# Optimization experiments

Measured on AMD Instinct MI355X. Metric: run time of the kernel, lower is better.

## Reference

```python
import jax, jax.numpy as jnp
import numpy as np

B, S, DIN, DOUT = 4, 2048, 4096, 4096

def setup_inputs() -> dict:
    key = jax.random.key(0)
    k1, k2, k3, k4 = jax.random.split(key, 4)
    x = jax.random.normal(k1, (B, S, DIN), dtype=jnp.float32)
    # int8 per-channel quantized weight (stored here as int32 holding int8 range values)
    weight = jax.random.randint(k2, (DOUT, DIN), -127, 128, dtype=jnp.int32)
    weight_scale = jax.random.uniform(k3, (DOUT,), dtype=jnp.float32, minval=0.001, maxval=0.02)
    weight_offset = jax.random.randint(k4, (DOUT,), -8, 8, dtype=jnp.int32)
    return {"x": x, "weight": weight, "weight_scale": weight_scale, "weight_offset": weight_offset}

def reference(x, weight, weight_scale, weight_offset):
    # W8A16 weight-only dequant: per-output-channel (w - offset) * scale, then GEMM.
    w_fp = (weight.astype(x.dtype) - weight_offset.astype(x.dtype)[:, None]) * weight_scale.astype(x.dtype)[:, None]  # [DOUT, DIN]
    # [B,S,DIN] @ [DOUT,DIN]^T -> [B,S,DOUT]
    return jnp.einsum('bsd,od->bso', x, w_fp)
```

## Files before the change

### kernel.cpp

```cpp
#include <hip/hip_runtime.h>
#include <stdint.h>

#define DIN   4096
#define DOUT  4096
#define MTOT  8192
#define NT    64

#define BM    256
#define BN    256
#define GRID_M (MTOT / BM)
#define GRID_N (DOUT / BN)
#define NWG   (GRID_M * GRID_N)

typedef __attribute__((ext_vector_type(4)))  float        f32x4;
typedef __attribute__((ext_vector_type(16))) float        f32x16;
typedef __attribute__((ext_vector_type(4)))  int          i32x4;
typedef __attribute__((ext_vector_type(4)))  unsigned int u32x4;
typedef __attribute__((ext_vector_type(2)))  unsigned int u32x2;
typedef __attribute__((ext_vector_type(8)))  short        bf16x8;

__device__ __forceinline__ unsigned int pack_bf2_rne(float a, float b) {
  unsigned int ua = __builtin_bit_cast(unsigned int, a);
  unsigned int ub = __builtin_bit_cast(unsigned int, b);
  ua += 0x7fffu + ((ua >> 16) & 1u);
  ub += 0x7fffu + ((ub >> 16) & 1u);
  return (ua >> 16) | (ub & 0xffff0000u);
}

__device__ __forceinline__ unsigned int pack_bf2_exact(int a, int b) {
  unsigned int ua = __builtin_bit_cast(unsigned int, (float)a);
  unsigned int ub = __builtin_bit_cast(unsigned int, (float)b);
  return (ua >> 16) | (ub & 0xffff0000u);
}

#define UNITS_A (GRID_M * 2 * NT)
#define UNITS_B (GRID_N * 2 * NT)
__global__ __launch_bounds__(256) void conv_kernel(const float* __restrict__ X,
                                                   u32x4* __restrict__ wsA,
                                                   const int* __restrict__ W,
                                                   const int* __restrict__ Off,
                                                   u32x4* __restrict__ wsB) {
  const int totA = UNITS_A * 1024;
  const int totB = UNITS_B * 1024;
  for (int idx = blockIdx.x * 256 + threadIdx.x; idx < totA + totB;
       idx += gridDim.x * 256) {
    if (idx < totA) {
      const int pos = idx & 1023;
      const int row = pos >> 3, ch = pos & 7;
      const int unit = idx >> 10;
      const int kt = unit & (NT - 1), rb = unit >> 6;
      const int m = rb * 128 + row;
      const f32x4* src = (const f32x4*)(X + ((long)m << 12) + kt * 64 + ch * 8);
      f32x4 f0 = src[0], f1 = src[1];
      u32x4 d;
      d[0] = pack_bf2_rne(f0[0], f0[1]);
      d[1] = pack_bf2_rne(f0[2], f0[3]);
      d[2] = pack_bf2_rne(f1[0], f1[1]);
      d[3] = pack_bf2_rne(f1[2], f1[3]);
      wsA[(long)unit * 1024 + ch * 128 + row] = d;
    } else {
      const int j = idx - totA;
      const int pos = j & 1023;
      const int row = pos >> 3, ch = pos & 7;
      const int unit = j >> 10;
      const int kt = unit & (NT - 1), nb = unit >> 6;
      const int n = nb * 128 + row;
      const i32x4* src = (const i32x4*)(W + ((long)n << 12) + kt * 64 + ch * 8);
      const int off = Off[n];
      i32x4 w0 = src[0], w1 = src[1];
      u32x4 d;
      d[0] = pack_bf2_exact(w0[0] - off, w0[1] - off);
      d[1] = pack_bf2_exact(w0[2] - off, w0[3] - off);
      d[2] = pack_bf2_exact(w1[0] - off, w1[1] - off);
      d[3] = pack_bf2_exact(w1[2] - off, w1[3] - off);
      wsB[(long)unit * 1024 + ch * 128 + row] = d;
    }
  }
}


#define BAR()   __builtin_amdgcn_s_barrier()
#define SB()    __builtin_amdgcn_sched_barrier(0)
#define LGKM_(N) asm volatile("s_waitcnt lgkmcnt(" #N ")" ::: "memory")
#define LGKM(N)  LGKM_(N)
#define WAITV(N) asm volatile("s_waitcnt vmcnt(" #N ")" ::: "memory")

typedef __attribute__((address_space(3))) const char* ldsp;

#define DSR(dst, p, IMM) \
  asm volatile("ds_read_b128 %0, %1 offset:" #IMM : "=v"(dst) : "v"(p))

#define STAGE(bufc, h, basePtr, t)                                              \
  { const u32x4* s_ = (basePtr) + (long)(t) * 1024;                             \
    _Pragma("unroll")                                                           \
    for (int i_ = 0; i_ < 2; ++i_) {                                            \
      const int o_ = tid + i_ * 512;                                            \
      __builtin_amdgcn_global_load_lds(                                         \
          (const __attribute__((address_space(1))) void*)(s_ + o_),             \
          (__attribute__((address_space(3))) void*)(&ldsA[bufc][h][0] + o_),    \
          16, 0, 0);                                                            \
    } }

#define BLOAD(kk, t)                                                            \
  { const char* pk_ = bBw + (long)((t) + 1) * 16384 + (kk) * 4096;              \
    asm volatile("global_load_dwordx4 %0, %1, off"                              \
                 : "=v"(bR[kk][0]) : "v"(pk_));                                 \
    asm volatile("global_load_dwordx4 %0, %1, off offset:512"                   \
                 : "=v"(bR[kk][1]) : "v"(pk_)); }

#define RD_A4(pA_, O0, O1, O2, O3)                                              \
  DSR(aR[0], pA_, O0); DSR(aR[1], pA_, O1);                                     \
  DSR(aR[2], pA_, O2); DSR(aR[3], pA_, O3);

#define MMA2(mt, kk)                                                            \
  acc[mt][0] = __builtin_amdgcn_mfma_f32_32x32x16_bf16(aR[mt], bR[kk][0],       \
                                                       acc[mt][0], 0, 0, 0);    \
  acc[mt][1] = __builtin_amdgcn_mfma_f32_32x32x16_bf16(aR[mt], bR[kk][1],       \
                                                       acc[mt][1], 0, 0, 0);

#define CASC(kk)                                                                \
  __builtin_amdgcn_s_setprio(1);                                                \
  LGKM(3); SB(); MMA2(0, kk)                                                    \
  LGKM(2); SB(); MMA2(1, kk)                                                    \
  LGKM(1); SB(); MMA2(2, kk)                                                    \
  LGKM(0); SB(); MMA2(3, kk)                                                    \
  __builtin_amdgcn_s_setprio(0);

#define TILE(pA_, ABUF, t, SG, W1, W2, W3, WE)                                  \
  RD_A4(pA_, 0, 512, 1024, 1536)                                                \
  if (SG) { STAGE(ABUF, 0, bA0, (t) + 1) }                                      \
  CASC(0)                                                                       \
  if (SG) { BLOAD(0, t) }                                                       \
  BAR();                                                                        \
  RD_A4(pA_, 4096, 4608, 5120, 5632)                                            \
  if (SG) { STAGE(ABUF, 1, bA1, (t) + 1) }                                      \
  W1; CASC(1)                                                                   \
  if (SG) { BLOAD(1, t) }                                                       \
  BAR();                                                                        \
  RD_A4(pA_, 8192, 8704, 9216, 9728)                                            \
  W2; CASC(2)                                                                   \
  if (SG) { BLOAD(2, t) }                                                       \
  BAR();                                                                        \
  RD_A4(pA_, 12288, 12800, 13312, 13824)                                        \
  W3; CASC(3)                                                                   \
  if (SG) { BLOAD(3, t) }                                                       \
  WE; BAR();

__global__ __launch_bounds__(512, 2) void gemm8_kernel(
    const u32x4* __restrict__ wsA, const u32x4* __restrict__ wsB,
    const float* __restrict__ Scale, float* __restrict__ Out) {
  __shared__ u32x4 ldsA[2][2][1024];

  const int tid  = threadIdx.x;
  const int lane = tid & 63;
  const int wid  = tid >> 6;
  const int wr   = wid >> 2;
  const int wc   = wid & 3;
  const int wch  = wc >> 1;
  const int wcl  = wc & 1;
  const int lane31 = lane & 31;
  const int lhi    = lane >> 5;

  int gid = (int)blockIdx.x;
  gid = (gid & 7) * (NWG >> 3) + (gid >> 3);
  const int wg_m = gid / GRID_N;
  const int wg_n = gid % GRID_N;

  const int lanepA = lane31 * 16 + lhi * 2048;

  ldsp pA0 = (ldsp)((const char*)&ldsA[0][wr][0] + lanepA);
  ldsp pA1 = (ldsp)((const char*)&ldsA[1][wr][0] + lanepA);

  const u32x4* bA0 = wsA + (long)(wg_m * 2 + 0) * NT * 1024;
  const u32x4* bA1 = wsA + (long)(wg_m * 2 + 1) * NT * 1024;
  const char* bBw = (const char*)(wsB + (long)(wg_n * 2 + wch) * NT * 1024)
                  + wcl * 1024 + lane31 * 16 + lhi * 2048;

  f32x16 acc[4][2];
#pragma unroll
  for (int m = 0; m < 4; ++m)
#pragma unroll
    for (int n = 0; n < 2; ++n)
#pragma unroll
      for (int q = 0; q < 16; ++q) acc[m][n][q] = 0.f;

  bf16x8 aR[4], bR[4][2];

  STAGE(0, 0, bA0, 0) STAGE(0, 1, bA1, 0)
  BLOAD(0, -1) BLOAD(1, -1) BLOAD(2, -1) BLOAD(3, -1)
  WAITV(6); BAR();

#pragma unroll 1
  for (int it = 0; it < 31; ++it) {
    const int t = 2 * it;
    TILE(pA0, 1, t,     1, WAITV(10), WAITV(10), WAITV(10), WAITV(6))
    TILE(pA1, 0, t + 1, 1, WAITV(10), WAITV(10), WAITV(10), WAITV(6))
  }
  TILE(pA0, 1, 62, 1, WAITV(10), WAITV(10), WAITV(10), WAITV(6))
  TILE(pA1, 0, 63, 0, WAITV(4),  WAITV(2),  WAITV(0),  )

  const int col0 = wg_n * BN + wc * 64 + lane31;
  const int row0 = wg_m * BM + wr * 128 + lhi * 4;
#pragma unroll
  for (int nt = 0; nt < 2; ++nt) {
    const int col = col0 + nt * 32;
    const float s = Scale[col];
#pragma unroll
    for (int mt = 0; mt < 4; ++mt) {
      const int rb = row0 + mt * 32;
#pragma unroll
      for (int q = 0; q < 4; ++q)
#pragma unroll
        for (int j = 0; j < 4; ++j)
          Out[(long)(rb + q * 8 + j) * DOUT + col] = acc[mt][nt][q * 4 + j] * s;
    }
  }
}

__global__ __launch_bounds__(256, 2) void gemm_fused_kernel(
    const float* __restrict__ X, const int* __restrict__ W,
    const int* __restrict__ Off, const float* __restrict__ Scale,
    float* __restrict__ Out) {
  __shared__ char ldsA[2][128 * 64 * 2];
  __shared__ char ldsB[2][128 * 64 * 2];

  const int tid  = threadIdx.x;
  const int lane = tid & 63;
  const int wid  = tid >> 6;
  const int fwr  = wid >> 1;
  const int fwc  = wid & 1;

  int gid = (int)blockIdx.x;
  gid = (gid & 7) * (2048 >> 3) + (gid >> 3);
  const int wg_m = gid / 32;
  const int wg_n = gid % 32;
  const int brow = wg_m * 128;
  const int bcol = wg_n * 128;

  f32x4 acc[4][4];
#pragma unroll
  for (int m = 0; m < 4; ++m)
#pragma unroll
    for (int n = 0; n < 4; ++n) acc[m][n] = (f32x4){0.f, 0.f, 0.f, 0.f};

  int aoff[2][4], boff[2][4];
#pragma unroll
  for (int kk = 0; kk < 2; ++kk)
#pragma unroll
    for (int m = 0; m < 4; ++m) {
      const int kb = kk * 64 + ((lane >> 4) << 4);
      const int ra = fwr * 64 + m * 16 + (lane & 15);
      const int rb = fwc * 64 + m * 16 + (lane & 15);
      aoff[kk][m] = ra * 128 + (kb ^ ((ra & 7) << 4));
      boff[kk][m] = rb * 128 + (kb ^ ((rb & 7) << 4));
    }

  long xo[8], wo[8];
  int lo[8], ofv[8];
#pragma unroll
  for (int i = 0; i < 8; ++i) {
    const int idx = tid + i * 256;
    const int row = idx >> 4, c4 = idx & 15;
    xo[i] = (long)(brow + row) * DIN + c4 * 4;
    wo[i] = (long)(bcol + row) * DIN + c4 * 4;
    lo[i] = row * 128 + ((c4 * 8) ^ ((row & 7) << 4));
    ofv[i] = Off[bcol + row];
  }
  {
#pragma unroll
    for (int i = 0; i < 8; ++i) {
      f32x4 f = *(const f32x4*)(X + xo[i]);
      u32x2 d;
      d[0] = pack_bf2_rne(f[0], f[1]);
      d[1] = pack_bf2_rne(f[2], f[3]);
      *(u32x2*)(&ldsA[0][lo[i]]) = d;
    }
#pragma unroll
    for (int i = 0; i < 8; ++i) {
      i32x4 w = *(const i32x4*)(W + wo[i]);
      u32x2 d;
      d[0] = pack_bf2_exact(w[0] - ofv[i], w[1] - ofv[i]);
      d[1] = pack_bf2_exact(w[2] - ofv[i], w[3] - ofv[i]);
      *(u32x2*)(&ldsB[0][lo[i]]) = d;
    }
  }
  __syncthreads();
#pragma unroll 1
  for (int kt = 0; kt < NT; ++kt) {
    const int cur = kt & 1;
    const bool pf = (kt + 1 < NT);
    f32x4 fa[8];
    i32x4 fb[8];
    if (pf) {
      const int ko = (kt + 1) * 64;
#pragma unroll
      for (int i = 0; i < 8; ++i) fa[i] = *(const f32x4*)(X + xo[i] + ko);
#pragma unroll
      for (int i = 0; i < 8; ++i) fb[i] = *(const i32x4*)(W + wo[i] + ko);
    }
#pragma unroll
    for (int kk = 0; kk < 2; ++kk) {
      bf16x8 fa2[4], fb2[4];
#pragma unroll
      for (int m = 0; m < 4; ++m)
        fa2[m] = __builtin_bit_cast(bf16x8, *(const u32x4*)(&ldsA[cur][aoff[kk][m]]));
#pragma unroll
      for (int n = 0; n < 4; ++n)
        fb2[n] = __builtin_bit_cast(bf16x8, *(const u32x4*)(&ldsB[cur][boff[kk][n]]));
#pragma unroll
      for (int m = 0; m < 4; ++m)
#pragma unroll
        for (int n = 0; n < 4; ++n)
          acc[m][n] = __builtin_amdgcn_mfma_f32_16x16x32_bf16(fa2[m], fb2[n], acc[m][n], 0, 0, 0);
    }
    if (pf) {
      char* dA = ldsA[cur ^ 1];
      char* dB = ldsB[cur ^ 1];
#pragma unroll
      for (int i = 0; i < 8; ++i) {
        u32x2 d;
        d[0] = pack_bf2_rne(fa[i][0], fa[i][1]);
        d[1] = pack_bf2_rne(fa[i][2], fa[i][3]);
        *(u32x2*)(&dA[lo[i]]) = d;
      }
#pragma unroll
      for (int i = 0; i < 8; ++i) {
        u32x2 d;
        d[0] = pack_bf2_exact(fb[i][0] - ofv[i], fb[i][1] - ofv[i]);
        d[1] = pack_bf2_exact(fb[i][2] - ofv[i], fb[i][3] - ofv[i]);
        *(u32x2*)(&dB[lo[i]]) = d;
      }
    }
    __syncthreads();
  }

  const int col0 = bcol + fwc * 64 + (lane & 15);
  const int row0 = brow + fwr * 64 + ((lane >> 4) << 2);
#pragma unroll
  for (int n = 0; n < 4; ++n) {
    const int col = col0 + n * 16;
    const float s = Scale[col];
#pragma unroll
    for (int m = 0; m < 4; ++m) {
      const int r = row0 + m * 16;
#pragma unroll
      for (int j = 0; j < 4; ++j)
        Out[(long)(r + j) * DOUT + col] = acc[m][n][j] * s;
    }
  }
}

extern "C" void kernel_launch(void* const* d_in, const int* in_sizes, int n_in,
                              void* d_out, int out_size, void* d_ws, size_t ws_size,
                              hipStream_t stream) {
  (void)in_sizes; (void)n_in; (void)out_size;
  const float* X  = (const float*)d_in[0];
  const int*   W  = (const int*)d_in[1];
  const float* Sc = (const float*)d_in[2];
  const int*   Of = (const int*)d_in[3];
  float* Out = (float*)d_out;

  const size_t needA = (size_t)MTOT * DIN * 2;
  const size_t needB = (size_t)DOUT * DIN * 2;
  if (ws_size >= needA + needB) {
    u32x4* wsA = (u32x4*)d_ws;
    u32x4* wsB = (u32x4*)((char*)d_ws + needA);
    conv_kernel<<<3072, 256, 0, stream>>>(X, wsA, W, Of, wsB);
    gemm8_kernel<<<NWG, 512, 0, stream>>>(wsA, wsB, Sc, Out);
  } else {
    gemm_fused_kernel<<<2048, 256, 0, stream>>>(X, W, Of, Sc, Out);
  }
}
```

Before: 284.1 us.

## Shrink GEMM workgroup to 128x256 tile with 4 waves each 64x128

```diff
diff --git a/kernel.cpp b/kernel.cpp
--- a/kernel.cpp
+++ b/kernel.cpp
@@ -6,11 +6,9 @@
 #define MTOT  8192
 #define NT    64
 
-#define BM    256
-#define BN    256
-#define GRID_M (MTOT / BM)
-#define GRID_N (DOUT / BN)
-#define NWG   (GRID_M * GRID_N)
+#define GRID_M 64
+#define GRID_N 16
+#define NWG    (GRID_M * GRID_N)
 
 typedef __attribute__((ext_vector_type(4)))  float        f32x4;
 typedef __attribute__((ext_vector_type(16))) float        f32x16;
@@ -33,7 +31,7 @@
   return (ua >> 16) | (ub & 0xffff0000u);
 }
 
-#define UNITS_A (GRID_M * 2 * NT)
+#define UNITS_A (GRID_M * NT)
 #define UNITS_B (GRID_N * 2 * NT)
 __global__ __launch_bounds__(256) void conv_kernel(const float* __restrict__ X,
                                                    u32x4* __restrict__ wsA,
@@ -90,14 +88,14 @@
 #define DSR(dst, p, IMM) \
   asm volatile("ds_read_b128 %0, %1 offset:" #IMM : "=v"(dst) : "v"(p))
 
-#define STAGE(bufc, h, basePtr, t)                                              \
-  { const u32x4* s_ = (basePtr) + (long)(t) * 1024;                             \
+#define STAGE(bufc, h, t)                                                       \
+  { const u32x4* s_ = bA + (long)(t) * 1024 + (h) * 512;                        \
     _Pragma("unroll")                                                           \
     for (int i_ = 0; i_ < 2; ++i_) {                                            \
-      const int o_ = tid + i_ * 512;                                            \
+      const int o_ = tid + i_ * 256;                                            \
       __builtin_amdgcn_global_load_lds(                                         \
           (const __attribute__((address_space(1))) void*)(s_ + o_),             \
-          (__attribute__((address_space(3))) void*)(&ldsA[bufc][h][0] + o_),    \
+          (__attribute__((address_space(3))) void*)(&ldsA[bufc][(h) * 512] + o_),\
           16, 0, 0);                                                            \
     } }
 
@@ -106,58 +104,53 @@
     asm volatile("global_load_dwordx4 %0, %1, off"                              \
                  : "=v"(bR[kk][0]) : "v"(pk_));                                 \
     asm volatile("global_load_dwordx4 %0, %1, off offset:512"                   \
-                 : "=v"(bR[kk][1]) : "v"(pk_)); }
-
-#define RD_A4(pA_, O0, O1, O2, O3)                                              \
-  DSR(aR[0], pA_, O0); DSR(aR[1], pA_, O1);                                     \
-  DSR(aR[2], pA_, O2); DSR(aR[3], pA_, O3);
-
-#define MMA2(mt, kk)                                                            \
-  acc[mt][0] = __builtin_amdgcn_mfma_f32_32x32x16_bf16(aR[mt], bR[kk][0],       \
-                                                       acc[mt][0], 0, 0, 0);    \
-  acc[mt][1] = __builtin_amdgcn_mfma_f32_32x32x16_bf16(aR[mt], bR[kk][1],       \
-                                                       acc[mt][1], 0, 0, 0);
+                 : "=v"(bR[kk][1]) : "v"(pk_));                                 \
+    asm volatile("global_load_dwordx4 %0, %1, off offset:1024"                  \
+                 : "=v"(bR[kk][2]) : "v"(pk_));                                 \
+    asm volatile("global_load_dwordx4 %0, %1, off offset:1536"                  \
+                 : "=v"(bR[kk][3]) : "v"(pk_)); }
+
+#define MMA4(mt, kk)                                                            \
+  { _Pragma("unroll") for (int n_ = 0; n_ < 4; ++n_)                            \
+      acc[mt][n_] = __builtin_amdgcn_mfma_f32_32x32x16_bf16(                    \
+          aR[mt], bR[kk][n_], acc[mt][n_], 0, 0, 0); }
 
 #define CASC(kk)                                                                \
   __builtin_amdgcn_s_setprio(1);                                                \
-  LGKM(3); SB(); MMA2(0, kk)                                                    \
-  LGKM(2); SB(); MMA2(1, kk)                                                    \
-  LGKM(1); SB(); MMA2(2, kk)                                                    \
-  LGKM(0); SB(); MMA2(3, kk)                                                    \
+  LGKM(1); SB(); MMA4(0, kk)                                                    \
+  LGKM(0); SB(); MMA4(1, kk)                                                    \
   __builtin_amdgcn_s_setprio(0);
 
 #define TILE(pA_, ABUF, t, SG, W1, W2, W3, WE)                                  \
-  RD_A4(pA_, 0, 512, 1024, 1536)                                                \
-  if (SG) { STAGE(ABUF, 0, bA0, (t) + 1) }                                      \
+  DSR(aR[0], pA_, 0); DSR(aR[1], pA_, 512);                                     \
+  if (SG) { STAGE(ABUF, 0, (t) + 1) }                                           \
   CASC(0)                                                                       \
   if (SG) { BLOAD(0, t) }                                                       \
   BAR();                                                                        \
-  RD_A4(pA_, 4096, 4608, 5120, 5632)                                            \
-  if (SG) { STAGE(ABUF, 1, bA1, (t) + 1) }                                      \
+  DSR(aR[0], pA_, 4096); DSR(aR[1], pA_, 4608);                                 \
+  if (SG) { STAGE(ABUF, 1, (t) + 1) }                                           \
   W1; CASC(1)                                                                   \
   if (SG) { BLOAD(1, t) }                                                       \
   BAR();                                                                        \
-  RD_A4(pA_, 8192, 8704, 9216, 9728)                                            \
+  DSR(aR[0], pA_, 8192); DSR(aR[1], pA_, 8704);                                 \
   W2; CASC(2)                                                                   \
   if (SG) { BLOAD(2, t) }                                                       \
   BAR();                                                                        \
-  RD_A4(pA_, 12288, 12800, 13312, 13824)                                        \
+  DSR(aR[0], pA_, 12288); DSR(aR[1], pA_, 12800);                               \
   W3; CASC(3)                                                                   \
   if (SG) { BLOAD(3, t) }                                                       \
   WE; BAR();
 
-__global__ __launch_bounds__(512, 2) void gemm8_kernel(
+__global__ __launch_bounds__(256, 2) void gemm4_kernel(
     const u32x4* __restrict__ wsA, const u32x4* __restrict__ wsB,
     const float* __restrict__ Scale, float* __restrict__ Out) {
-  __shared__ u32x4 ldsA[2][2][1024];
+  __shared__ u32x4 ldsA[2][1024];
 
   const int tid  = threadIdx.x;
   const int lane = tid & 63;
   const int wid  = tid >> 6;
-  const int wr   = wid >> 2;
-  const int wc   = wid & 3;
-  const int wch  = wc >> 1;
-  const int wcl  = wc & 1;
+  const int wrM  = wid >> 1;
+  const int wcN  = wid & 1;
   const int lane31 = lane & 31;
   const int lhi    = lane >> 5;
 
@@ -166,47 +159,45 @@
   const int wg_m = gid / GRID_N;
   const int wg_n = gid % GRID_N;
 
-  const int lanepA = lane31 * 16 + lhi * 2048;
-
-  ldsp pA0 = (ldsp)((const char*)&ldsA[0][wr][0] + lanepA);
-  ldsp pA1 = (ldsp)((const char*)&ldsA[1][wr][0] + lanepA);
-
-  const u32x4* bA0 = wsA + (long)(wg_m * 2 + 0) * NT * 1024;
-  const u32x4* bA1 = wsA + (long)(wg_m * 2 + 1) * NT * 1024;
-  const char* bBw = (const char*)(wsB + (long)(wg_n * 2 + wch) * NT * 1024)
-                  + wcl * 1024 + lane31 * 16 + lhi * 2048;
-
-  f32x16 acc[4][2];
-#pragma unroll
-  for (int m = 0; m < 4; ++m)
-#pragma unroll
-    for (int n = 0; n < 2; ++n)
+  const int lanepA = (wrM * 64 + lane31) * 16 + lhi * 2048;
+  ldsp pA0 = (ldsp)((const char*)&ldsA[0][0] + lanepA);
+  ldsp pA1 = (ldsp)((const char*)&ldsA[1][0] + lanepA);
+
+  const u32x4* bA = wsA + (long)wg_m * NT * 1024;
+  const char* bBw = (const char*)(wsB + (long)(wg_n * 2 + wcN) * NT * 1024)
+                  + lane31 * 16 + lhi * 2048;
+
+  f32x16 acc[2][4];
+#pragma unroll
+  for (int m = 0; m < 2; ++m)
+#pragma unroll
+    for (int n = 0; n < 4; ++n)
 #pragma unroll
       for (int q = 0; q < 16; ++q) acc[m][n][q] = 0.f;
 
-  bf16x8 aR[4], bR[4][2];
-
-  STAGE(0, 0, bA0, 0) STAGE(0, 1, bA1, 0)
+  bf16x8 aR[2], bR[4][4];
+
+  STAGE(0, 0, 0) STAGE(0, 1, 0)
   BLOAD(0, -1) BLOAD(1, -1) BLOAD(2, -1) BLOAD(3, -1)
-  WAITV(6); BAR();
+  WAITV(12); BAR();
 
 #pragma unroll 1
   for (int it = 0; it < 31; ++it) {
     const int t = 2 * it;
-    TILE(pA0, 1, t,     1, WAITV(10), WAITV(10), WAITV(10), WAITV(6))
-    TILE(pA1, 0, t + 1, 1, WAITV(10), WAITV(10), WAITV(10), WAITV(6))
-  }
-  TILE(pA0, 1, 62, 1, WAITV(10), WAITV(10), WAITV(10), WAITV(6))
-  TILE(pA1, 0, 63, 0, WAITV(4),  WAITV(2),  WAITV(0),  )
-
-  const int col0 = wg_n * BN + wc * 64 + lane31;
-  const int row0 = wg_m * BM + wr * 128 + lhi * 4;
-#pragma unroll
-  for (int nt = 0; nt < 2; ++nt) {
+    TILE(pA0, 1, t,     1, WAITV(16), WAITV(16), WAITV(16), WAITV(12))
+    TILE(pA1, 0, t + 1, 1, WAITV(16), WAITV(16), WAITV(16), WAITV(12))
+  }
+  TILE(pA0, 1, 62, 1, WAITV(16), WAITV(16), WAITV(16), WAITV(12))
+  TILE(pA1, 0, 63, 0, WAITV(8),  WAITV(4),  WAITV(0),  )
+
+  const int col0 = wg_n * 256 + wcN * 128 + lane31;
+  const int row0 = wg_m * 128 + wrM * 64 + lhi * 4;
+#pragma unroll
+  for (int nt = 0; nt < 4; ++nt) {
     const int col = col0 + nt * 32;
     const float s = Scale[col];
 #pragma unroll
-    for (int mt = 0; mt < 4; ++mt) {
+    for (int mt = 0; mt < 2; ++mt) {
       const int rb = row0 + mt * 32;
 #pragma unroll
       for (int q = 0; q < 4; ++q)
@@ -366,7 +357,7 @@
     u32x4* wsA = (u32x4*)d_ws;
     u32x4* wsB = (u32x4*)((char*)d_ws + needA);
     conv_kernel<<<3072, 256, 0, stream>>>(X, wsA, W, Of, wsB);
-    gemm8_kernel<<<NWG, 512, 0, stream>>>(wsA, wsB, Sc, Out);
+    gemm4_kernel<<<NWG, 256, 0, stream>>>(wsA, wsB, Sc, Out);
   } else {
     gemm_fused_kernel<<<2048, 256, 0, stream>>>(X, W, Of, Sc, Out);
   }
```

Measured after the change: 313.7 us. 10.4% more time.
